# Performance work log

Measured on AMD Instinct MI355X. Metric: run time of the kernel, lower is better.

Reference implementation:

```python
import jax, jax.numpy as jnp
import numpy as np

EMBED = 256
NHEAD = 8
DFF = 1024
NLAYERS = 1
B, H, W, WS = 4, 128, 128, 16


def _layernorm(x, g, b, eps=1e-5):
    mu = jnp.mean(x, axis=-1, keepdims=True)
    var = jnp.var(x, axis=-1, keepdims=True)
    return (x - mu) * jax.lax.rsqrt(var + eps) * g + b


def _mha(q, k, v, in_w, in_b, out_w, out_b, kpm=None):
    # torch nn.MultiheadAttention (batch_first) with dropout=0
    Bn, L, C = q.shape
    dh = C // NHEAD
    wq, wk, wv = jnp.split(in_w, 3, axis=0)
    bq, bk, bv = jnp.split(in_b, 3, axis=0)
    qh = (q @ wq.T + bq).reshape(Bn, L, NHEAD, dh)
    kh = (k @ wk.T + bk).reshape(Bn, k.shape[1], NHEAD, dh)
    vh = (v @ wv.T + bv).reshape(Bn, v.shape[1], NHEAD, dh)
    scores = jnp.einsum('bqhd,bkhd->bhqk', qh, kh) * (dh ** -0.5)
    if kpm is not None:  # True == masked key
        scores = jnp.where(kpm[:, None, None, :], -jnp.inf, scores)
    attn = jax.nn.softmax(scores, axis=-1)
    out = jnp.einsum('bhqk,bkhd->bqhd', attn, vh).reshape(Bn, L, C)
    return out @ out_w.T + out_b


def _enc_layer(q, k, v, p, kpm=None):
    # post-norm AxisPermutedEncoderLayer, dropout=0
    (in_w, in_b, out_w, out_b, l1w, l1b, l2w, l2b, g1, b1, g2, b2) = p
    src = v + _mha(q, k, v, in_w, in_b, out_w, out_b, kpm)
    src = _layernorm(src, g1, b1)
    ff = jax.nn.relu(src @ l1w.T + l1b) @ l2w.T + l2b
    return _layernorm(src + ff, g2, b2)


def _forward(backbone_memory, defe_feature_filtered, window_size, glob_pos_embed,
             rel_w1, rel_b1, rel_w2, rel_b2,
             in_proj_w, in_proj_b, out_proj_w, out_proj_b,
             lin1_w, lin1_b, lin2_w, lin2_b, ln1_g, ln1_b, ln2_g, ln2_b):
    Bb, C, Hh, Ww = backbone_memory.shape
    ws = window_size
    nwh, nww = Hh // ws, Ww // ws
    nw, T = nwh * nww, ws * ws
    p = (in_proj_w, in_proj_b, out_proj_w, out_proj_b,
         lin1_w, lin1_b, lin2_w, lin2_b, ln1_g, ln1_b, ln2_g, ln2_b)
    # relative position embedding: MLP over normalized in-window (y,x) coords
    ys, xs = jnp.meshgrid(jnp.arange(ws), jnp.arange(ws), indexing='ij')
    coords = jnp.stack([ys, xs], -1).reshape(T, 2).astype(backbone_memory.dtype) / max(ws - 1, 1)
    rel = jax.nn.relu(coords @ rel_w1.T + rel_b1) @ rel_w2.T + rel_b2  # [T,C]
    # window partition -> [B, nw, T, C]
    feats = backbone_memory.reshape(Bb, C, nwh, ws, nww, ws).transpose(0, 2, 4, 1, 3, 5)
    feats = feats.reshape(Bb, nw, C, T).transpose(0, 1, 3, 2)
    gp = glob_pos_embed.reshape(C, nwh, ws, nww, ws).transpose(1, 3, 0, 2, 4)
    gp = gp.reshape(nw, C, T).transpose(0, 2, 1)[None]  # [1,nw,T,C]
    pos = jnp.broadcast_to(gp + rel[None, None], (Bb, nw, T, C))
    # window validity via max-pool of binary map
    pooled = defe_feature_filtered.reshape(Bb, 1, nwh, ws, nww, ws).max(axis=(3, 5))
    valid = pooled.reshape(Bb, nw) > 0  # bool [B,nw]
    x = feats
    for _ in range(NLAYERS):
        # within-window attention over T tokens
        wi = x.reshape(Bb * nw, T, C)
        wp = pos.reshape(Bb * nw, T, C)
        x = _enc_layer(wi + wp, wi + wp, wi, p).reshape(Bb, nw, T, C)
        # cross-window attention over nw windows (per token position)
        ci = x.transpose(0, 2, 1, 3).reshape(Bb * T, nw, C)
        cp = pos.transpose(0, 2, 1, 3).reshape(Bb * T, nw, C)
        kpm = jnp.broadcast_to(~valid[:, None, :], (Bb, T, nw)).reshape(Bb * T, nw)
        x = _enc_layer(ci + cp, ci + cp, ci, p, kpm).reshape(Bb, T, nw, C).transpose(0, 2, 1, 3)
    enc = x.transpose(0, 1, 3, 2).reshape(Bb, nw, C, ws, ws)
    enc = enc * valid.astype(x.dtype)[:, :, None, None, None]
    upd = enc.reshape(Bb, nwh, nww, C, ws, ws).transpose(0, 3, 1, 4, 2, 5).reshape(Bb, C, Hh, Ww)
    return backbone_memory + upd, valid


def setup_inputs() -> dict:
    key = jax.random.key(0)
    ks = jax.random.split(key, 16)
    C, s = EMBED, 0.02
    inp = {}
    inp['backbone_memory'] = jax.random.normal(ks[0], (B, C, H, W), jnp.float32)
    inp['defe_feature_filtered'] = (jax.random.uniform(ks[1], (B, 1, H, W)) < 0.002).astype(jnp.float32)
    inp['window_size'] = WS
    inp['glob_pos_embed'] = jax.random.normal(ks[2], (C, H, W), jnp.float32) * s
    inp['rel_w1'] = jax.random.normal(ks[3], (64, 2), jnp.float32) * s
    inp['rel_b1'] = jnp.zeros((64,), jnp.float32)
    inp['rel_w2'] = jax.random.normal(ks[4], (C, 64), jnp.float32) * s
    inp['rel_b2'] = jnp.zeros((C,), jnp.float32)
    inp['in_proj_w'] = jax.random.normal(ks[5], (3 * C, C), jnp.float32) * s
    inp['in_proj_b'] = jnp.zeros((3 * C,), jnp.float32)
    inp['out_proj_w'] = jax.random.normal(ks[6], (C, C), jnp.float32) * s
    inp['out_proj_b'] = jnp.zeros((C,), jnp.float32)
    inp['lin1_w'] = jax.random.normal(ks[7], (DFF, C), jnp.float32) * s
    inp['lin1_b'] = jnp.zeros((DFF,), jnp.float32)
    inp['lin2_w'] = jax.random.normal(ks[8], (C, DFF), jnp.float32) * s
    inp['lin2_b'] = jnp.zeros((C,), jnp.float32)
    inp['ln1_g'] = jnp.ones((C,), jnp.float32)
    inp['ln1_b'] = jnp.zeros((C,), jnp.float32)
    inp['ln2_g'] = jnp.ones((C,), jnp.float32)
    inp['ln2_b'] = jnp.zeros((C,), jnp.float32)
    return inp


def reference(backbone_memory, defe_feature_filtered, window_size, glob_pos_embed,
              rel_w1, rel_b1, rel_w2, rel_b2,
              in_proj_w, in_proj_b, out_proj_w, out_proj_b,
              lin1_w, lin1_b, lin2_w, lin2_b, ln1_g, ln1_b, ln2_g, ln2_b):
    return _forward(backbone_memory, defe_feature_filtered, window_size, glob_pos_embed,
                    rel_w1, rel_b1, rel_w2, rel_b2,
                    in_proj_w, in_proj_b, out_proj_w, out_proj_b,
                    lin1_w, lin1_b, lin2_w, lin2_b, ln1_g, ln1_b, ln2_g, ln2_b)
```

## Files before the change

kernel.cpp:

```cpp
#include <hip/hip_runtime.h>
#include <hip/hip_bf16.h>

#define CEMB 256
#define NHEAD 8
#define DHEAD 32
#define DFF 1024
#define BB 4
#define HH 128
#define WW 128
#define WSZ 16
#define NWH 8
#define NW 64
#define TT 256
#define NTOK (BB*NW*TT)

typedef __attribute__((ext_vector_type(8))) short bf16x8;
typedef __attribute__((ext_vector_type(4))) float f32x4;

__device__ __forceinline__ float bf2f(unsigned short u){
    union { float f; unsigned int i; } v; v.i = ((unsigned int)u) << 16; return v.f;
}
__device__ __forceinline__ unsigned short f2bf(float f){
    union { float f; unsigned int i; } v; v.f = f;
    unsigned int r = v.i + 0x7fffu + ((v.i >> 16) & 1u);
    return (unsigned short)(r >> 16);
}
__device__ __forceinline__ unsigned int cvtpk_bf16(float lo, float hi){
    unsigned int r;
    asm("v_cvt_pk_bf16_f32 %0, %1, %2" : "=v"(r) : "v"(lo), "v"(hi));
    return r;
}
__device__ __forceinline__ void unpack8(uint4 v, float* f){
    f[0]=bf2f((unsigned short)(v.x & 0xffff)); f[1]=bf2f((unsigned short)(v.x>>16));
    f[2]=bf2f((unsigned short)(v.y & 0xffff)); f[3]=bf2f((unsigned short)(v.y>>16));
    f[4]=bf2f((unsigned short)(v.z & 0xffff)); f[5]=bf2f((unsigned short)(v.z>>16));
    f[6]=bf2f((unsigned short)(v.w & 0xffff)); f[7]=bf2f((unsigned short)(v.w>>16));
}
__device__ __forceinline__ void async_copy16(const void* g, void* l){
    __builtin_amdgcn_global_load_lds(
        (const __attribute__((address_space(1))) unsigned int*)g,
        (__attribute__((address_space(3))) unsigned int*)l, 16, 0, 0);
}
__device__ __forceinline__ int sgran(int c, int g){ return c*32 + (g ^ (c & 31)); }

__global__ __launch_bounds__(256) void rel_kernel(const float* __restrict__ rw1,
    const float* __restrict__ rb1, const float* __restrict__ rw2,
    const float* __restrict__ rb2, float* __restrict__ rel)
{
    __shared__ float hsh[64];
    int t = blockIdx.x, c = threadIdx.x;
    int ty = t >> 4, tx = t & 15;
    if (c < 64){
        float y = ty*(1.0f/15.0f), xx = tx*(1.0f/15.0f);
        hsh[c] = fmaxf(y*rw1[2*c] + xx*rw1[2*c+1] + rb1[c], 0.0f);
    }
    __syncthreads();
    float acc = rb2[c];
    #pragma unroll 16
    for (int k = 0; k < 64; ++k) acc += hsh[k]*rw2[c*64 + k];
    rel[t*256 + c] = acc;
}

__global__ __launch_bounds__(256) void posT_kernel(const float* __restrict__ gp,
    const float* __restrict__ rel, unsigned short* __restrict__ pos)
{
    __shared__ float tile[8192];
    const int w  = blockIdx.x >> 3;
    const int cq = (blockIdx.x >> 1) & 3, th = blockIdx.x & 1;
    const int c0 = cq << 6, t0 = th << 7, y0 = th << 3;
    const int wh = w >> 3, wwi = w & 7;
    const int tid = threadIdx.x;
    const float* gpb = gp + (size_t)c0*(HH*WW) + (size_t)(wh*16 + y0)*WW + wwi*16;
    #pragma unroll
    for (int i = 0; i < 8; ++i){
        int n = i*256 + tid, slot = n & 31, c = n >> 5;
        int yl = slot >> 2, xg = slot & 3;
        float4 v = *(const float4*)(gpb + (size_t)c*(HH*WW) + yl*WW + xg*4);
        *(float4*)&tile[sgran(c, slot)*4] = v;
    }
    __syncthreads();
    #pragma unroll
    for (int i = 0; i < 4; ++i){
        int n = i*256 + tid, j = n & 7, tl = n >> 3;
        int g = tl >> 2, e = tl & 3;
        const float* rl = rel + (t0 + tl)*256 + c0 + j*8;
        unsigned short o[8];
        #pragma unroll
        for (int m = 0; m < 8; ++m)
            o[m] = f2bf(tile[sgran(j*8 + m, g)*4 + e] + rl[m]);
        *(uint4*)&pos[((size_t)w*256 + t0 + tl)*CEMB + c0 + j*8] = *(uint4*)o;
    }
}

__global__ __launch_bounds__(256) void valid_kernel(const float* __restrict__ defe,
    float* __restrict__ validf, float* __restrict__ tail)
{
    __shared__ float red[4];
    int bw = blockIdx.x; int b = bw >> 6, w = bw & 63;
    int t = threadIdx.x; int ty = t >> 4, tx = t & 15;
    int wh = w >> 3, wwi = w & 7;
    float v = defe[(size_t)b*(HH*WW) + (wh*16+ty)*WW + wwi*16 + tx];
    int lane = t & 63, wave = t >> 6;
    for (int off = 1; off < 64; off <<= 1) v = fmaxf(v, __shfl_xor(v, off));
    if (lane == 0) red[wave] = v;
    __syncthreads();
    if (t == 0){
        float m = fmaxf(fmaxf(red[0], red[1]), fmaxf(red[2], red[3]));
        float r = (m > 0.0f) ? 1.0f : 0.0f;
        validf[bw] = r;
        tail[bw] = r;
    }
}

__global__ __launch_bounds__(256) void partition_kernel(const float* __restrict__ bb,
    unsigned short* __restrict__ x)
{
    __shared__ float tile[8192];
    const int bw = blockIdx.x >> 3;
    const int b = bw >> 6, w = bw & 63;
    const int cq = (blockIdx.x >> 1) & 3, th = blockIdx.x & 1;
    const int c0 = cq << 6, t0 = th << 7, y0 = th << 3;
    const int wh = w >> 3, wwi = w & 7;
    const int tid = threadIdx.x;
    const float* bbb = bb + ((size_t)(b*CEMB + c0))*(HH*WW) + (size_t)(wh*16 + y0)*WW + wwi*16;
    #pragma unroll
    for (int i = 0; i < 8; ++i){
        int n = i*256 + tid, slot = n & 31, c = n >> 5;
        int yl = slot >> 2, xg = slot & 3;
        float4 v = *(const float4*)(bbb + (size_t)c*(HH*WW) + yl*WW + xg*4);
        *(float4*)&tile[sgran(c, slot)*4] = v;
    }
    __syncthreads();
    #pragma unroll
    for (int i = 0; i < 4; ++i){
        int n = i*256 + tid, j = n & 7, tl = n >> 3;
        int g = tl >> 2, e = tl & 3;
        unsigned short o[8];
        #pragma unroll
        for (int m = 0; m < 8; ++m)
            o[m] = f2bf(tile[sgran(j*8 + m, g)*4 + e]);
        *(uint4*)&x[((size_t)bw*256 + t0 + tl)*CEMB + c0 + j*8] = *(uint4*)o;
    }
}

__global__ __launch_bounds__(256) void wcvt_kernel(const float* __restrict__ w,
    unsigned short* __restrict__ o, int n4)
{
    int i = blockIdx.x*256 + threadIdx.x;
    if (i < n4){
        float4 v = ((const float4*)w)[i];
        ushort4 u;
        u.x = f2bf(v.x); u.y = f2bf(v.y); u.z = f2bf(v.z); u.w = f2bf(v.w);
        ((ushort4*)o)[i] = u;
    }
}

__global__ __launch_bounds__(256) void addpos_kernel(const unsigned short* __restrict__ x,
    const unsigned short* __restrict__ pos, unsigned short* __restrict__ xp)
{
    size_t i = ((size_t)blockIdx.x*256 + threadIdx.x) * 8;
    size_t tok = i >> 8; int c = (int)(i & 255);
    size_t pi = ((tok & 16383) << 8) + c;
    uint4 xv = *(const uint4*)&x[i];
    uint4 pv = *(const uint4*)&pos[pi];
    float xf[8], pf[8]; unpack8(xv, xf); unpack8(pv, pf);
    unsigned short o[8];
    #pragma unroll
    for (int j = 0; j < 8; ++j) o[j] = f2bf(xf[j] + pf[j]);
    *(uint4*)&xp[i] = *(uint4*)o;
}

__global__ __launch_bounds__(256) void gemm_mfma(
    const unsigned short* __restrict__ A,
    const unsigned short* __restrict__ A2, int nsplit, int ldA,
    const unsigned short* __restrict__ W, int K,
    const float* __restrict__ bias,
    unsigned short* __restrict__ out, int ldO, int relu)
{
    __shared__ unsigned short As[128*32];
    __shared__ unsigned short Bs[128*32];
    const int m0 = blockIdx.x << 7, n0 = blockIdx.y << 7;
    const int tid = threadIdx.x;
    const int lane = tid & 63, wave = tid >> 6;
    const int wm = wave & 1, wn = wave >> 1;
    const int fl = lane & 15, quad = lane >> 4;

    const unsigned short* Ap = ((n0 < nsplit) ? A : A2) + (size_t)m0*ldA;
    const unsigned short* Wp = W + (size_t)n0*K;

    const int c0 = tid, c1 = tid + 256;
    const int r0 = c0 >> 2, o0 = ((c0 & 3) ^ ((c0 >> 3) & 3)) << 3;
    const int r1 = c1 >> 2, o1 = ((c1 & 3) ^ ((c1 >> 3) & 3)) << 3;
    const int sw = (quad ^ ((fl >> 1) & 3)) << 3;

    f32x4 acc[4][4] = {};

    for (int k0 = 0; k0 < K; k0 += 32){
        async_copy16(Ap + (size_t)r0*ldA + k0 + o0, &As[c0 << 3]);
        async_copy16(Ap + (size_t)r1*ldA + k0 + o1, &As[c1 << 3]);
        async_copy16(Wp + (size_t)r0*K   + k0 + o0, &Bs[c0 << 3]);
        async_copy16(Wp + (size_t)r1*K   + k0 + o1, &Bs[c1 << 3]);
        __syncthreads();
        bf16x8 av[4], bv[4];
        #pragma unroll
        for (int i = 0; i < 4; ++i){
            av[i] = *(const bf16x8*)&As[(wm*64 + i*16 + fl)*32 + sw];
            bv[i] = *(const bf16x8*)&Bs[(wn*64 + i*16 + fl)*32 + sw];
        }
        #pragma unroll
        for (int i = 0; i < 4; ++i)
            #pragma unroll
            for (int j = 0; j < 4; ++j)
                acc[i][j] = __builtin_amdgcn_mfma_f32_16x16x32_bf16(av[i], bv[j], acc[i][j], 0, 0, 0);
        __syncthreads();
    }

    float bj[4];
    #pragma unroll
    for (int j = 0; j < 4; ++j) bj[j] = bias[n0 + wn*64 + j*16 + fl];
    #pragma unroll
    for (int i = 0; i < 4; ++i){
        int mrow = m0 + wm*64 + i*16 + quad*4;
        #pragma unroll
        for (int j = 0; j < 4; ++j){
            int col = n0 + wn*64 + j*16 + fl;
            #pragma unroll
            for (int r = 0; r < 4; ++r){
                float v = acc[i][j][r] + bj[j];
                if (relu) v = fmaxf(v, 0.0f);
                out[(size_t)(mrow + r)*ldO + col] = f2bf(v);
            }
        }
    }
}

__global__ __launch_bounds__(256, 3) void gemm_ln(
    const unsigned short* __restrict__ A, int K,
    const unsigned short* __restrict__ W,
    const float* __restrict__ bias,
    const unsigned short* __restrict__ resid,
    const float* __restrict__ g, const float* __restrict__ b,
    unsigned short* __restrict__ out)
{
    __shared__ unsigned short As[64*32];
    __shared__ unsigned short Bs[256*32];
    __shared__ float psum[4][64];
    __shared__ float psq[4][64];
    const int m0 = blockIdx.x << 6;
    const int tid = threadIdx.x, lane = tid & 63, wave = tid >> 6;
    const int wn = wave;
    const int fl = lane & 15, quad = lane >> 4;

    const unsigned short* Ap = A + (size_t)m0*K;

    const int ra = tid >> 2, oa = ((tid & 3) ^ ((tid >> 3) & 3)) << 3;
    const int sw = (quad ^ ((fl >> 1) & 3)) << 3;

    f32x4 acc[4][4] = {};

    for (int k0 = 0; k0 < K; k0 += 32){
        async_copy16(Ap + (size_t)ra*K + k0 + oa, &As[tid << 3]);
        #pragma unroll
        for (int t = 0; t < 4; ++t){
            int c = tid + t*256;
            int r = c >> 2, o = ((c & 3) ^ ((c >> 3) & 3)) << 3;
            async_copy16(W + (size_t)r*K + k0 + o, &Bs[c << 3]);
        }
        __syncthreads();
        bf16x8 av[4], bv[4];
        #pragma unroll
        for (int i = 0; i < 4; ++i)
            av[i] = *(const bf16x8*)&As[(i*16 + fl)*32 + sw];
        #pragma unroll
        for (int j = 0; j < 4; ++j)
            bv[j] = *(const bf16x8*)&Bs[(wn*64 + j*16 + fl)*32 + sw];
        #pragma unroll
        for (int i = 0; i < 4; ++i)
            #pragma unroll
            for (int j = 0; j < 4; ++j)
                acc[i][j] = __builtin_amdgcn_mfma_f32_16x16x32_bf16(av[i], bv[j], acc[i][j], 0, 0, 0);
        __syncthreads();
    }

    float bcol[4], gcol[4], bbcol[4];
    #pragma unroll
    for (int j = 0; j < 4; ++j){
        int col = wn*64 + j*16 + fl;
        bcol[j] = bias[col]; gcol[j] = g[col]; bbcol[j] = b[col];
    }
    float s[4][4] = {{0}}, sq[4][4] = {{0}};
    #pragma unroll
    for (int i = 0; i < 4; ++i)
        #pragma unroll
        for (int r = 0; r < 4; ++r){
            int row = m0 + i*16 + quad*4 + r;
            #pragma unroll
            for (int j = 0; j < 4; ++j){
                float h = acc[i][j][r] + bcol[j]
                        + bf2f(resid[(size_t)row*256 + wn*64 + j*16 + fl]);
                acc[i][j][r] = h;
                s[i][r] += h; sq[i][r] += h*h;
            }
        }
    #pragma unroll
    for (int i = 0; i < 4; ++i)
        #pragma unroll
        for (int r = 0; r < 4; ++r){
            float ss = s[i][r], qq = sq[i][r];
            ss += __shfl_xor(ss, 1); qq += __shfl_xor(qq, 1);
            ss += __shfl_xor(ss, 2); qq += __shfl_xor(qq, 2);
            ss += __shfl_xor(ss, 4); qq += __shfl_xor(qq, 4);
            ss += __shfl_xor(ss, 8); qq += __shfl_xor(qq, 8);
            if (fl == 0){
                int lr = i*16 + quad*4 + r;
                psum[wn][lr] = ss; psq[wn][lr] = qq;
            }
        }
    __syncthreads();
    #pragma unroll
    for (int i = 0; i < 4; ++i)
        #pragma unroll
        for (int r = 0; r < 4; ++r){
            int lr = i*16 + quad*4 + r;
            float mu  = (psum[0][lr] + psum[1][lr] + psum[2][lr] + psum[3][lr]) * (1.0f/256.0f);
            float var = (psq[0][lr] + psq[1][lr] + psq[2][lr] + psq[3][lr]) * (1.0f/256.0f) - mu*mu;
            float rstd = rsqrtf(var + 1e-5f);
            #pragma unroll
            for (int j = 0; j < 4; ++j){
                int col = wn*64 + j*16 + fl;
                out[(size_t)(m0 + lr)*256 + col] =
                    f2bf((acc[i][j][r] - mu)*rstd*gcol[j] + bbcol[j]);
            }
        }
}

__global__ __launch_bounds__(256, 2) void ffn_fused(
    const unsigned short* __restrict__ src,
    const unsigned short* __restrict__ w1,
    const float* __restrict__ b1,
    const unsigned short* __restrict__ w2,
    const float* __restrict__ b2,
    const float* __restrict__ g, const float* __restrict__ b,
    unsigned short* __restrict__ out)
{
    __shared__ unsigned short w1buf[64*256];
    __shared__ unsigned short w2buf[256*64];
    __shared__ unsigned short hlds[64*64];
    __shared__ float psum[4][64];
    __shared__ float psq[4][64];
    const int m0 = blockIdx.x << 6;
    const int tid = threadIdx.x, lane = tid & 63, wave = tid >> 6;
    const int fl = lane & 15, quad = lane >> 4;
    const int fsl = fl & 7;

    bf16x8 qf[4][8];
    #pragma unroll
    for (int mi = 0; mi < 4; ++mi)
        #pragma unroll
        for (int kf = 0; kf < 8; ++kf)
            qf[mi][kf] = *(const bf16x8*)&src[(size_t)(m0 + mi*16 + fl)*256 + kf*32 + quad*8];

    f32x4 acc[4][4] = {};
    const int gwr = wave*2 + (quad >> 1);
    const int who = (quad & 1) << 2;

    #pragma unroll
    for (int i = 0; i < 8; ++i){
        int G = i*256 + tid, hid = G >> 5, gp = G & 31;
        async_copy16(w1 + (size_t)hid*256 + ((gp ^ (hid & 7)) << 3), &w1buf[G << 3]);
    }
    __syncthreads();

    for (int c = 0; c < 16; ++c){
        const int j0 = c << 6;
        #pragma unroll
        for (int i = 0; i < 8; ++i){
            int G = i*256 + tid, oc = G >> 3, gp = G & 7;
            async_copy16(w2 + (size_t)oc*1024 + j0 + ((gp ^ (oc & 7)) << 3), &w2buf[G << 3]);
        }
        bf16x8 w1f[8];
        #pragma unroll
        for (int kf = 0; kf < 8; ++kf)
            w1f[kf] = *(const bf16x8*)&w1buf[(((wave*16 + fl) << 5) + ((kf*4 + quad) ^ fsl)) << 3];
        float4 b1v = *(const float4*)&b1[j0 + wave*16 + quad*4];
        #pragma unroll
        for (int mi = 0; mi < 4; ++mi){
            f32x4 sacc = {};
            #pragma unroll
            for (int kf = 0; kf < 8; ++kf)
                sacc = __builtin_amdgcn_mfma_f32_16x16x32_bf16(w1f[kf], qf[mi][kf], sacc, 0, 0, 0);
            float h0 = fmaxf(sacc[0] + b1v.x, 0.0f);
            float h1 = fmaxf(sacc[1] + b1v.y, 0.0f);
            float h2 = fmaxf(sacc[2] + b1v.z, 0.0f);
            float h3 = fmaxf(sacc[3] + b1v.w, 0.0f);
            int r_ = mi*16 + fl;
            int gb = r_*64 + ((gwr ^ fsl) << 3) + who;
            *(unsigned int*)&hlds[gb    ] = cvtpk_bf16(h0, h1);
            *(unsigned int*)&hlds[gb + 2] = cvtpk_bf16(h2, h3);
        }
        __syncthreads();
        if (c < 15){
            #pragma unroll
            for (int i = 0; i < 8; ++i){
                int G = i*256 + tid, hid = G >> 5, gp = G & 31;
                async_copy16(w1 + (size_t)(j0 + 64 + hid)*256 + ((gp ^ (hid & 7)) << 3), &w1buf[G << 3]);
            }
        }
        #pragma unroll
        for (int kk = 0; kk < 2; ++kk){
            bf16x8 hf[4], w2f[4];
            #pragma unroll
            for (int mi = 0; mi < 4; ++mi)
                hf[mi] = *(const bf16x8*)&hlds[(mi*16 + fl)*64 + (((kk*4 + quad) ^ fsl) << 3)];
            #pragma unroll
            for (int nd = 0; nd < 4; ++nd)
                w2f[nd] = *(const bf16x8*)&w2buf[(((wave*64 + nd*16 + fl) << 3) + ((kk*4 + quad) ^ fsl)) << 3];
            #pragma unroll
            for (int mi = 0; mi < 4; ++mi)
                #pragma unroll
                for (int nd = 0; nd < 4; ++nd)
                    acc[mi][nd] = __builtin_amdgcn_mfma_f32_16x16x32_bf16(hf[mi], w2f[nd], acc[mi][nd], 0, 0, 0);
        }
        __syncthreads();
    }

    float bcol[4], gcol[4], bbcol[4];
    #pragma unroll
    for (int j = 0; j < 4; ++j){
        int col = wave*64 + j*16 + fl;
        bcol[j] = b2[col]; gcol[j] = g[col]; bbcol[j] = b[col];
    }
    float s[4][4] = {{0}}, sq[4][4] = {{0}};
    #pragma unroll
    for (int i = 0; i < 4; ++i)
        #pragma unroll
        for (int r = 0; r < 4; ++r){
            int row = m0 + i*16 + quad*4 + r;
            #pragma unroll
            for (int j = 0; j < 4; ++j){
                float h = acc[i][j][r] + bcol[j]
                        + bf2f(src[(size_t)row*256 + wave*64 + j*16 + fl]);
                acc[i][j][r] = h;
                s[i][r] += h; sq[i][r] += h*h;
            }
        }
    #pragma unroll
    for (int i = 0; i < 4; ++i)
        #pragma unroll
        for (int r = 0; r < 4; ++r){
            float ss = s[i][r], qq = sq[i][r];
            ss += __shfl_xor(ss, 1); qq += __shfl_xor(qq, 1);
            ss += __shfl_xor(ss, 2); qq += __shfl_xor(qq, 2);
            ss += __shfl_xor(ss, 4); qq += __shfl_xor(qq, 4);
            ss += __shfl_xor(ss, 8); qq += __shfl_xor(qq, 8);
            if (fl == 0){
                int lr = i*16 + quad*4 + r;
                psum[wave][lr] = ss; psq[wave][lr] = qq;
            }
        }
    __syncthreads();
    #pragma unroll
    for (int i = 0; i < 4; ++i)
        #pragma unroll
        for (int r = 0; r < 4; ++r){
            int lr = i*16 + quad*4 + r;
            float mu  = (psum[0][lr] + psum[1][lr] + psum[2][lr] + psum[3][lr]) * (1.0f/256.0f);
            float var = (psq[0][lr] + psq[1][lr] + psq[2][lr] + psq[3][lr]) * (1.0f/256.0f) - mu*mu;
            float rstd = rsqrtf(var + 1e-5f);
            #pragma unroll
            for (int j = 0; j < 4; ++j){
                int col = wave*64 + j*16 + fl;
                out[(size_t)(m0 + lr)*256 + col] =
                    f2bf((acc[i][j][r] - mu)*rstd*gcol[j] + bbcol[j]);
            }
        }
}

template<int L, bool CROSS>
__global__ __launch_bounds__(256, 3) void attn_mfma(const unsigned short* __restrict__ qkv,
    unsigned short* __restrict__ attn_out, const float* __restrict__ validf)
{
    constexpr int QW  = (L == 256) ? 64 : 16;
    constexpr int MI  = QW / 16;
    constexpr int VTS = L + 8;
    constexpr int LOG = (L == 256) ? 8 : 6;
    __shared__ unsigned short Ks[L*32];
    __shared__ unsigned short Vt[32*VTS];

    const int s = blockIdx.x, h = blockIdx.y;
    int base, stride;
    if (CROSS){ base = (s >> 8)*16384 + (s & 255); stride = 256; }
    else      { base = s << 8; stride = 1; }
    const int tid = threadIdx.x, lane = tid & 63, wave = tid >> 6;
    const int fl = lane & 15, quad = lane >> 4;
    const float scale = 0.17677669529663687f;

    for (int cid = tid; cid < L*4; cid += 256){
        int j = cid >> 2, part = (cid & 3) ^ ((cid >> 3) & 3);
        async_copy16(qkv + (size_t)(base + j*stride)*768 + 256 + h*32 + part*8, &Ks[cid*8]);
    }
    for (int e = tid; e < L*4; e += 256){
        int j = e & (L-1), dp = e >> LOG;
        uint4 vv = *(const uint4*)(qkv + (size_t)(base + j*stride)*768 + 512 + h*32 + dp*8);
        unsigned short tmp[8]; *(uint4*)tmp = vv;
        #pragma unroll
        for (int d = 0; d < 8; ++d) Vt[(dp*8 + d)*VTS + j] = tmp[d];
    }
    __syncthreads();

    bf16x8 qf[MI];
    #pragma unroll
    for (int mi = 0; mi < MI; ++mi){
        int q = wave*QW + mi*16 + fl;
        qf[mi] = *(const bf16x8*)(qkv + (size_t)(base + q*stride)*768 + h*32 + quad*8);
    }
    float vm[4][4];
    if (CROSS){
        #pragma unroll
        for (int nj = 0; nj < 4; ++nj){
            float4 v4 = *(const float4*)&validf[(s >> 8)*64 + nj*16 + quad*4];
            vm[nj][0] = v4.x; vm[nj][1] = v4.y; vm[nj][2] = v4.z; vm[nj][3] = v4.w;
        }
    }

    f32x4 oacc[MI][2] = {};
    float lpart[MI] = {};
    const int sw = (quad ^ ((fl >> 1) & 3)) << 3;
    const int la = fl | ((quad & 1) << 5);
    const int lb = la + 16;

    for (int j0 = 0; j0 < L; j0 += 64){
        bf16x8 kf[4];
        #pragma unroll
        for (int nj = 0; nj < 4; ++nj)
            kf[nj] = *(const bf16x8*)&Ks[(j0 + nj*16 + fl)*32 + sw];
        unsigned int pk[MI][4][2];
        #pragma unroll
        for (int mi = 0; mi < MI; ++mi){
            f32x4 sacc[4] = {};
            #pragma unroll
            for (int nj = 0; nj < 4; ++nj)
                sacc[nj] = __builtin_amdgcn_mfma_f32_16x16x32_bf16(kf[nj], qf[mi], sacc[nj], 0, 0, 0);
            #pragma unroll
            for (int nj = 0; nj < 4; ++nj){
                float p[4];
                #pragma unroll
                for (int r = 0; r < 4; ++r){
                    float pv = __expf(sacc[nj][r] * scale);
                    if (CROSS) pv *= vm[nj][r];
                    p[r] = pv;
                    lpart[mi] += pv;
                }
                pk[mi][nj][0] = cvtpk_bf16(p[0], p[1]);
                pk[mi][nj][1] = cvtpk_bf16(p[2], p[3]);
            }
        }
        #pragma unroll
        for (int kk = 0; kk < 2; ++kk){
            bf16x8 vf[2];
            #pragma unroll
            for (int nd = 0; nd < 2; ++nd)
                vf[nd] = *(const bf16x8*)&Vt[(nd*16 + fl)*VTS + j0 + kk*32 + quad*8];
            #pragma unroll
            for (int mi = 0; mi < MI; ++mi){
                unsigned int a0 = __shfl(pk[mi][2*kk  ][0], la, 64);
                unsigned int a1 = __shfl(pk[mi][2*kk  ][1], la, 64);
                unsigned int a2 = __shfl(pk[mi][2*kk  ][0], lb, 64);
                unsigned int a3 = __shfl(pk[mi][2*kk  ][1], lb, 64);
                unsigned int b0 = __shfl(pk[mi][2*kk+1][0], la, 64);
                unsigned int b1 = __shfl(pk[mi][2*kk+1][1], la, 64);
                unsigned int b2 = __shfl(pk[mi][2*kk+1][0], lb, 64);
                unsigned int b3 = __shfl(pk[mi][2*kk+1][1], lb, 64);
                const bool lo = quad < 2;
                union { unsigned int u[4]; bf16x8 v; } pu;
                pu.u[0] = lo ? a0 : b0;
                pu.u[1] = lo ? a1 : b1;
                pu.u[2] = lo ? a2 : b2;
                pu.u[3] = lo ? a3 : b3;
                #pragma unroll
                for (int nd = 0; nd < 2; ++nd)
                    oacc[mi][nd] = __builtin_amdgcn_mfma_f32_16x16x32_bf16(pu.v, vf[nd], oacc[mi][nd], 0, 0, 0);
            }
        }
    }

    #pragma unroll
    for (int mi = 0; mi < MI; ++mi){
        float l = lpart[mi];
        l += __shfl_xor(l, 16);
        l += __shfl_xor(l, 32);
        l = 1.0f / l;
        float li[4];
        #pragma unroll
        for (int r = 0; r < 4; ++r)
            li[r] = __shfl(l, quad*4 + r, 64);
        #pragma unroll
        for (int nd = 0; nd < 2; ++nd)
            #pragma unroll
            for (int r = 0; r < 4; ++r){
                int q = wave*QW + mi*16 + quad*4 + r;
                attn_out[(size_t)(base + q*stride)*CEMB + h*32 + nd*16 + fl] =
                    f2bf(oacc[mi][nd][r] * li[r]);
            }
    }
}

__global__ __launch_bounds__(256) void scatter_kernel(const float* __restrict__ bb,
    const unsigned short* __restrict__ x, const float* __restrict__ validf,
    float* __restrict__ out)
{
    __shared__ float tile[8192];
    const int bw = blockIdx.x >> 3;
    const int b = bw >> 6, w = bw & 63;
    const int cq = (blockIdx.x >> 1) & 3, th = blockIdx.x & 1;
    const int c0 = cq << 6, t0 = th << 7, y0 = th << 3;
    const int wh = w >> 3, wwi = w & 7;
    const int tid = threadIdx.x;
    const float vf = validf[bw];
    #pragma unroll
    for (int i = 0; i < 4; ++i){
        int n = i*256 + tid, j = n & 7, tl = n >> 3;
        int g = tl >> 2, e = tl & 3;
        uint4 xv = *(const uint4*)&x[((size_t)bw*256 + t0 + tl)*CEMB + c0 + j*8];
        float f[8]; unpack8(xv, f);
        #pragma unroll
        for (int m = 0; m < 8; ++m)
            tile[sgran(j*8 + m, g)*4 + e] = f[m];
    }
    __syncthreads();
    const size_t gbase = ((size_t)(b*CEMB + c0))*(HH*WW) + (size_t)(wh*16 + y0)*WW + wwi*16;
    #pragma unroll
    for (int i = 0; i < 8; ++i){
        int n = i*256 + tid, slot = n & 31, c = n >> 5;
        int yl = slot >> 2, xg = slot & 3;
        size_t gi = gbase + (size_t)c*(HH*WW) + yl*WW + xg*4;
        float4 bv = *(const float4*)(bb + gi);
        float4 xv = *(const float4*)&tile[sgran(c, slot)*4];
        float4 ov;
        ov.x = bv.x + vf*xv.x; ov.y = bv.y + vf*xv.y;
        ov.z = bv.z + vf*xv.z; ov.w = bv.w + vf*xv.w;
        *(float4*)(out + gi) = ov;
    }
}

extern "C" void kernel_launch(void* const* d_in, const int* in_sizes, int n_in,
                              void* d_out, int out_size, void* d_ws, size_t ws_size,
                              hipStream_t stream)
{
    (void)in_sizes; (void)n_in; (void)out_size; (void)ws_size;
    const float* backbone = (const float*)d_in[0];
    const float* defe     = (const float*)d_in[1];
    const float* gpe      = (const float*)d_in[3];
    const float* rw1 = (const float*)d_in[4];
    const float* rb1 = (const float*)d_in[5];
    const float* rw2 = (const float*)d_in[6];
    const float* rb2 = (const float*)d_in[7];
    const float* ipw = (const float*)d_in[8];
    const float* ipb = (const float*)d_in[9];
    const float* opw = (const float*)d_in[10];
    const float* opb = (const float*)d_in[11];
    const float* l1w = (const float*)d_in[12];
    const float* l1b = (const float*)d_in[13];
    const float* l2w = (const float*)d_in[14];
    const float* l2b = (const float*)d_in[15];
    const float* g1  = (const float*)d_in[16];
    const float* b1  = (const float*)d_in[17];
    const float* g2  = (const float*)d_in[18];
    const float* b2  = (const float*)d_in[19];

    char* ws = (char*)d_ws;
    unsigned short* pos    = (unsigned short*)(ws);
    unsigned short* x      = (unsigned short*)(ws +   8388608);
    unsigned short* qkv    = (unsigned short*)(ws +  41943040);
    unsigned short* shared_= (unsigned short*)(ws + 142606336);
    float*          validf = (float*)(ws + 176160768);
    unsigned short* ipw16  = (unsigned short*)(ws + 176161792);
    unsigned short* opw16  = (unsigned short*)(ws + 176555008);
    unsigned short* l1w16  = (unsigned short*)(ws + 176686080);
    unsigned short* l2w16  = (unsigned short*)(ws + 177210368);
    float*          rel    = (float*)(ws + 177734656);
    unsigned short* src = qkv;
    float* outf = (float*)d_out;

    wcvt_kernel<<<192, 256, 0, stream>>>(ipw, ipw16, 49152);
    wcvt_kernel<<< 64, 256, 0, stream>>>(opw, opw16, 16384);
    wcvt_kernel<<<256, 256, 0, stream>>>(l1w, l1w16, 65536);
    wcvt_kernel<<<256, 256, 0, stream>>>(l2w, l2w16, 65536);
    rel_kernel<<<256, 256, 0, stream>>>(rw1, rb1, rw2, rb2, rel);
    posT_kernel<<<512, 256, 0, stream>>>(gpe, rel, pos);
    valid_kernel<<<BB*NW, 256, 0, stream>>>(defe, validf, outf + (size_t)BB*CEMB*HH*WW);
    partition_kernel<<<2048, 256, 0, stream>>>(backbone, x);

    for (int layer = 0; layer < 2; ++layer){
        addpos_kernel<<<8192, 256, 0, stream>>>(x, pos, shared_);
        gemm_mfma<<<dim3(512, 6), 256, 0, stream>>>(shared_, x, 512, CEMB, ipw16, CEMB, ipb, qkv, 768, 0);
        if (layer == 0)
            attn_mfma<256, false><<<dim3(BB*NW, NHEAD), 256, 0, stream>>>(qkv, shared_, validf);
        else
            attn_mfma<64, true><<<dim3(BB*TT, NHEAD), 256, 0, stream>>>(qkv, shared_, validf);
        gemm_ln<<<dim3(1024, 1), 256, 0, stream>>>(shared_, CEMB, opw16, opb, x, g1, b1, src);
        ffn_fused<<<1024, 256, 0, stream>>>(src, l1w16, l1b, l2w16, l2b, g2, b2, x);
    }
    scatter_kernel<<<2048, 256, 0, stream>>>(backbone, x, validf, outf);
}
```

Baseline: 800.8 us.

## Pre-shuffle FFN weights into MFMA fragment order and load directly to registers

New one-time kernels convert lin1/lin2 weights to bf16 already arranged in per-lane MFMA fragment order. The fused FFN kernel then loads weight fragments straight from global memory into registers, prefetching the next chunk instead of staging through LDS. The activation tile now goes to LDS via async copies and is read from there for both the first GEMM and the residual add. This shrinks LDS use, which may let more blocks fit per CU, and removes the LDS weight round-trips. The cost is more register pressure and global-load latency exposed inside the loop.

```diff
diff --git a/kernel.cpp b/kernel.cpp
--- a/kernel.cpp
+++ b/kernel.cpp
@@ -155,6 +155,32 @@
     }
 }
 
+__global__ __launch_bounds__(256) void wshuf1_kernel(const float* __restrict__ w,
+    unsigned short* __restrict__ o)
+{
+    int n = blockIdx.x*256 + threadIdx.x;
+    int l = n & 63, kf = (n >> 6) & 7, wv = (n >> 9) & 3, c = n >> 11;
+    int row = c*64 + wv*16 + (l & 15), col = kf*32 + (l >> 4)*8;
+    const float* s = w + (size_t)row*256 + col;
+    unsigned short u[8];
+    #pragma unroll
+    for (int e = 0; e < 8; ++e) u[e] = f2bf(s[e]);
+    *(uint4*)&o[(size_t)n*8] = *(uint4*)u;
+}
+
+__global__ __launch_bounds__(256) void wshuf2_kernel(const float* __restrict__ w,
+    unsigned short* __restrict__ o)
+{
+    int n = blockIdx.x*256 + threadIdx.x;
+    int l = n & 63, nd = (n >> 6) & 3, wv = (n >> 8) & 3, kk = (n >> 10) & 1, c = n >> 11;
+    int row = wv*64 + nd*16 + (l & 15), col = c*64 + kk*32 + (l >> 4)*8;
+    const float* s = w + (size_t)row*1024 + col;
+    unsigned short u[8];
+    #pragma unroll
+    for (int e = 0; e < 8; ++e) u[e] = f2bf(s[e]);
+    *(uint4*)&o[(size_t)n*8] = *(uint4*)u;
+}
+
 __global__ __launch_bounds__(256) void addpos_kernel(const unsigned short* __restrict__ x,
     const unsigned short* __restrict__ pos, unsigned short* __restrict__ xp)
 {
@@ -336,15 +362,14 @@
 
 __global__ __launch_bounds__(256, 2) void ffn_fused(
     const unsigned short* __restrict__ src,
-    const unsigned short* __restrict__ w1,
+    const unsigned short* __restrict__ w1r,
     const float* __restrict__ b1,
-    const unsigned short* __restrict__ w2,
+    const unsigned short* __restrict__ w2r,
     const float* __restrict__ b2,
     const float* __restrict__ g, const float* __restrict__ b,
     unsigned short* __restrict__ out)
 {
-    __shared__ unsigned short w1buf[64*256];
-    __shared__ unsigned short w2buf[256*64];
+    __shared__ unsigned short slds[64*256];
     __shared__ unsigned short hlds[64*64];
     __shared__ float psum[4][64];
     __shared__ float psq[4][64];
@@ -353,42 +378,43 @@
     const int fl = lane & 15, quad = lane >> 4;
     const int fsl = fl & 7;
 
-    bf16x8 qf[4][8];
-    #pragma unroll
-    for (int mi = 0; mi < 4; ++mi)
-        #pragma unroll
-        for (int kf = 0; kf < 8; ++kf)
-            qf[mi][kf] = *(const bf16x8*)&src[(size_t)(m0 + mi*16 + fl)*256 + kf*32 + quad*8];
+    #pragma unroll
+    for (int i = 0; i < 8; ++i){
+        int G = i*256 + tid, row = G >> 5, gp = G & 31;
+        async_copy16(src + (size_t)(m0 + row)*256 + ((gp ^ (row & 7)) << 3), &slds[G << 3]);
+    }
+    asm volatile("s_waitcnt vmcnt(0)" ::: "memory");
+    __builtin_amdgcn_sched_barrier(0);
+    __builtin_amdgcn_s_barrier();
 
     f32x4 acc[4][4] = {};
     const int gwr = wave*2 + (quad >> 1);
     const int who = (quad & 1) << 2;
 
-    #pragma unroll
-    for (int i = 0; i < 8; ++i){
-        int G = i*256 + tid, hid = G >> 5, gp = G & 31;
-        async_copy16(w1 + (size_t)hid*256 + ((gp ^ (hid & 7)) << 3), &w1buf[G << 3]);
-    }
-    __syncthreads();
-
+    bf16x8 w1f[8], w2f[2][4];
+    #pragma unroll
+    for (int kf = 0; kf < 8; ++kf)
+        w1f[kf] = *(const bf16x8*)&w1r[(size_t)((wave*8 + kf)*64 + lane)*8];
+    #pragma unroll
+    for (int kk = 0; kk < 2; ++kk)
+        #pragma unroll
+        for (int nd = 0; nd < 4; ++nd)
+            w2f[kk][nd] = *(const bf16x8*)&w2r[(size_t)(((kk*4 + wave)*4 + nd)*64 + lane)*8];
+
+    #pragma unroll 1
     for (int c = 0; c < 16; ++c){
         const int j0 = c << 6;
-        #pragma unroll
-        for (int i = 0; i < 8; ++i){
-            int G = i*256 + tid, oc = G >> 3, gp = G & 7;
-            async_copy16(w2 + (size_t)oc*1024 + j0 + ((gp ^ (oc & 7)) << 3), &w2buf[G << 3]);
-        }
-        bf16x8 w1f[8];
-        #pragma unroll
-        for (int kf = 0; kf < 8; ++kf)
-            w1f[kf] = *(const bf16x8*)&w1buf[(((wave*16 + fl) << 5) + ((kf*4 + quad) ^ fsl)) << 3];
         float4 b1v = *(const float4*)&b1[j0 + wave*16 + quad*4];
         #pragma unroll
         for (int mi = 0; mi < 4; ++mi){
+            bf16x8 qf[8];
+            #pragma unroll
+            for (int kf = 0; kf < 8; ++kf)
+                qf[kf] = *(const bf16x8*)&slds[((mi*16 + fl)*32 + ((kf*4 + quad) ^ fsl)) << 3];
             f32x4 sacc = {};
             #pragma unroll
             for (int kf = 0; kf < 8; ++kf)
-                sacc = __builtin_amdgcn_mfma_f32_16x16x32_bf16(w1f[kf], qf[mi][kf], sacc, 0, 0, 0);
+                sacc = __builtin_amdgcn_mfma_f32_16x16x32_bf16(w1f[kf], qf[kf], sacc, 0, 0, 0);
             float h0 = fmaxf(sacc[0] + b1v.x, 0.0f);
             float h1 = fmaxf(sacc[1] + b1v.y, 0.0f);
             float h2 = fmaxf(sacc[2] + b1v.z, 0.0f);
@@ -398,30 +424,38 @@
             *(unsigned int*)&hlds[gb    ] = cvtpk_bf16(h0, h1);
             *(unsigned int*)&hlds[gb + 2] = cvtpk_bf16(h2, h3);
         }
-        __syncthreads();
         if (c < 15){
             #pragma unroll
-            for (int i = 0; i < 8; ++i){
-                int G = i*256 + tid, hid = G >> 5, gp = G & 31;
-                async_copy16(w1 + (size_t)(j0 + 64 + hid)*256 + ((gp ^ (hid & 7)) << 3), &w1buf[G << 3]);
-            }
-        }
+            for (int kf = 0; kf < 8; ++kf)
+                w1f[kf] = *(const bf16x8*)&w1r[(size_t)((((c+1)*4 + wave)*8 + kf)*64 + lane)*8];
+        }
+        asm volatile("s_waitcnt lgkmcnt(0)" ::: "memory");
+        __builtin_amdgcn_sched_barrier(0);
+        __builtin_amdgcn_s_barrier();
+        __builtin_amdgcn_sched_barrier(0);
         #pragma unroll
         for (int kk = 0; kk < 2; ++kk){
-            bf16x8 hf[4], w2f[4];
+            bf16x8 hf[4];
             #pragma unroll
             for (int mi = 0; mi < 4; ++mi)
                 hf[mi] = *(const bf16x8*)&hlds[(mi*16 + fl)*64 + (((kk*4 + quad) ^ fsl) << 3)];
-            #pragma unroll
-            for (int nd = 0; nd < 4; ++nd)
-                w2f[nd] = *(const bf16x8*)&w2buf[(((wave*64 + nd*16 + fl) << 3) + ((kk*4 + quad) ^ fsl)) << 3];
             #pragma unroll
             for (int mi = 0; mi < 4; ++mi)
                 #pragma unroll
                 for (int nd = 0; nd < 4; ++nd)
-                    acc[mi][nd] = __builtin_amdgcn_mfma_f32_16x16x32_bf16(hf[mi], w2f[nd], acc[mi][nd], 0, 0, 0);
-        }
-        __syncthreads();
+                    acc[mi][nd] = __builtin_amdgcn_mfma_f32_16x16x32_bf16(hf[mi], w2f[kk][nd], acc[mi][nd], 0, 0, 0);
+        }
+        if (c < 15){
+            #pragma unroll
+            for (int kk = 0; kk < 2; ++kk)
+                #pragma unroll
+                for (int nd = 0; nd < 4; ++nd)
+                    w2f[kk][nd] = *(const bf16x8*)&w2r[(size_t)(((((c+1)*2 + kk)*4 + wave)*4 + nd)*64 + lane)*8];
+        }
+        asm volatile("s_waitcnt lgkmcnt(0)" ::: "memory");
+        __builtin_amdgcn_sched_barrier(0);
+        __builtin_amdgcn_s_barrier();
+        __builtin_amdgcn_sched_barrier(0);
     }
 
     float bcol[4], gcol[4], bbcol[4];
@@ -435,11 +469,12 @@
     for (int i = 0; i < 4; ++i)
         #pragma unroll
         for (int r = 0; r < 4; ++r){
-            int row = m0 + i*16 + quad*4 + r;
+            int lr = i*16 + quad*4 + r;
             #pragma unroll
             for (int j = 0; j < 4; ++j){
-                float h = acc[i][j][r] + bcol[j]
-                        + bf2f(src[(size_t)row*256 + wave*64 + j*16 + fl]);
+                int gcol2 = wave*8 + j*2 + (fl >> 3);
+                float rv = bf2f(slds[((lr*32 + (gcol2 ^ (lr & 7))) << 3) + (fl & 7)]);
+                float h = acc[i][j][r] + bcol[j] + rv;
                 acc[i][j][r] = h;
                 s[i][r] += h; sq[i][r] += h*h;
             }
@@ -676,16 +711,16 @@
     float*          validf = (float*)(ws + 176160768);
     unsigned short* ipw16  = (unsigned short*)(ws + 176161792);
     unsigned short* opw16  = (unsigned short*)(ws + 176555008);
-    unsigned short* l1w16  = (unsigned short*)(ws + 176686080);
-    unsigned short* l2w16  = (unsigned short*)(ws + 177210368);
+    unsigned short* w1r    = (unsigned short*)(ws + 176686080);
+    unsigned short* w2r    = (unsigned short*)(ws + 177210368);
     float*          rel    = (float*)(ws + 177734656);
     unsigned short* src = qkv;
     float* outf = (float*)d_out;
 
     wcvt_kernel<<<192, 256, 0, stream>>>(ipw, ipw16, 49152);
     wcvt_kernel<<< 64, 256, 0, stream>>>(opw, opw16, 16384);
-    wcvt_kernel<<<256, 256, 0, stream>>>(l1w, l1w16, 65536);
-    wcvt_kernel<<<256, 256, 0, stream>>>(l2w, l2w16, 65536);
+    wshuf1_kernel<<<128, 256, 0, stream>>>(l1w, w1r);
+    wshuf2_kernel<<<128, 256, 0, stream>>>(l2w, w2r);
     rel_kernel<<<256, 256, 0, stream>>>(rw1, rb1, rw2, rb2, rel);
     posT_kernel<<<512, 256, 0, stream>>>(gpe, rel, pos);
     valid_kernel<<<BB*NW, 256, 0, stream>>>(defe, validf, outf + (size_t)BB*CEMB*HH*WW);
@@ -699,7 +734,7 @@
         else
             attn_mfma<64, true><<<dim3(BB*TT, NHEAD), 256, 0, stream>>>(qkv, shared_, validf);
         gemm_ln<<<dim3(1024, 1), 256, 0, stream>>>(shared_, CEMB, opw16, opb, x, g1, b1, src);
-        ffn_fused<<<1024, 256, 0, stream>>>(src, l1w16, l1b, l2w16, l2b, g2, b2, x);
+        ffn_fused<<<1024, 256, 0, stream>>>(src, w1r, l1b, w2r, l2b, g2, b2, x);
     }
     scatter_kernel<<<2048, 256, 0, stream>>>(backbone, x, validf, outf);
 }
```

Measured after the change: 674.2 us. 15.8% less time.
